# Kernel optimization log

Hardware: AMD Instinct MI355X
Metric: run time of the kernel (lower is better)

Reference implementation:

```python
import jax, jax.numpy as jnp
import numpy as np
from jax import lax
from jax.scipy.special import logsumexp

LOG2PI = 1.8378770664093453

def _gauss_lp(x, mean, logvar):
    return -0.5 * ((x - mean) ** 2 * jnp.exp(-logvar) + logvar + LOG2PI)

def setup_inputs() -> dict:
    key = jax.random.key(0)
    ks = jax.random.split(key, 12)
    B, T, D, H, X, K, U = 32, 1024, 512, 512, 32, 8, 2
    s = 0.05
    return {
        'ys': jax.random.normal(ks[0], (B, T, D), jnp.float32),
        'us': jax.random.normal(ks[1], (B, T, U), jnp.float32),
        'eps': jax.random.normal(ks[2], (B, T, X), jnp.float32),
        'W1': jax.random.normal(ks[3], (D, H), jnp.float32) * s,
        'b1': jnp.zeros((H,), jnp.float32),
        'Wmu': jax.random.normal(ks[4], (H, X), jnp.float32) * s,
        'bmu': jnp.zeros((X,), jnp.float32),
        'Wlv': jax.random.normal(ks[5], (H, X), jnp.float32) * s,
        'blv': jnp.zeros((X,), jnp.float32),
        'Wz': jax.random.normal(ks[6], (X, K * K), jnp.float32) * s,
        'bz': jnp.zeros((K * K,), jnp.float32),
        'A': jax.random.normal(ks[7], (K, X, X), jnp.float32) * s,
        'Bu': jax.random.normal(ks[8], (K, U, X), jnp.float32) * s,
        'bx': jnp.zeros((K, X), jnp.float32),
        'x_logvar': jnp.zeros((K, X), jnp.float32),
        'x0_mean': jax.random.normal(ks[9], (K, X), jnp.float32) * s,
        'x0_logvar': jnp.zeros((K, X), jnp.float32),
        'C': jax.random.normal(ks[10], (X, D), jnp.float32) * s,
        'd': jnp.zeros((D,), jnp.float32),
        'y_logvar': jnp.zeros((D,), jnp.float32),
        'log_init_z': jnp.zeros((K,), jnp.float32),
    }

def _forward_backward(log_a, log_b, log_init):
    # log_a: [B,T,K,K] with log_a[:,t,j,k] = log p(z_t=j | z_{t-1}=k); log_b: [B,T,K]
    B, T, K = log_b.shape
    la = jnp.moveaxis(log_a[:, 1:], 1, 0)  # [T-1,B,K,K]
    lb = jnp.moveaxis(log_b[:, 1:], 1, 0)  # [T-1,B,K]
    a0 = log_init[None, :] + log_b[:, 0]
    c0 = logsumexp(a0, axis=-1)
    a0 = a0 - c0[:, None]
    def fstep(alpha, ab):
        la_t, lb_t = ab
        a = lb_t + logsumexp(la_t + alpha[:, None, :], axis=-1)
        c = logsumexp(a, axis=-1)
        an = a - c[:, None]
        return an, (an, c)
    _, (alphas, cs) = lax.scan(fstep, a0, (la, lb))
    log_px = c0 + jnp.sum(cs, axis=0)  # [B] log marginal likelihood
    fwd = jnp.concatenate([a0[None], alphas], axis=0)  # [T,B,K]
    betaT = jnp.zeros((B, K), log_b.dtype)
    def bstep(beta, ab):
        la_t, lb_t = ab
        b = logsumexp(la_t + (lb_t + beta)[:, :, None], axis=1)  # sum over next-state j
        b = b - logsumexp(b, axis=-1, keepdims=True)
        return b, b
    _, betas = lax.scan(bstep, betaT, (la, lb), reverse=True)
    bwd = jnp.concatenate([betas, betaT[None]], axis=0)  # [T,B,K]
    lg = fwd + bwd
    log_gamma1 = lg - logsumexp(lg, axis=-1, keepdims=True)
    return jnp.moveaxis(log_gamma1, 0, 1), log_px

def reference(ys, us, eps, W1, b1, Wmu, bmu, Wlv, blv, Wz, bz, A, Bu, bx,
              x_logvar, x0_mean, x0_logvar, C, d, y_logvar, log_init_z):
    B, T, D = ys.shape
    K, X = x0_mean.shape
    # inference net q(x|y): per-step MLP producing Gaussian, reparameterized sample
    h = jnp.tanh(ys @ W1 + b1)
    mu = h @ Wmu + bmu
    lv = h @ Wlv + blv
    x = mu + jnp.exp(0.5 * lv) * eps                        # [B,T,X]
    x_entropy = 0.5 * jnp.sum(eps ** 2 + lv + LOG2PI, -1)   # -log q(x^), [B,T]
    # discrete transition log p(z_t | z_{t-1}, x_{t-1}) with log(eye) prepended at t=0
    logits = (x[:, :-1] @ Wz + bz).reshape(B, T - 1, K, K)
    log_a_t = jax.nn.log_softmax(logits, axis=-2)           # normalize_logprob axis=-2
    log_eye = jnp.log(jnp.eye(K, dtype=ys.dtype) + 1e-10)[None, None]
    log_a = jnp.concatenate([jnp.broadcast_to(log_eye, (B, 1, K, K)), log_a_t], axis=1)
    # continuous likelihood log p(x_t | x_{t-1}, u_t, z_t=k) -> [B,T,K]
    log_b0 = jnp.sum(_gauss_lp(x[:, 0, None, :], x0_mean, x0_logvar), -1)  # [B,K]
    means = (jnp.einsum('btd,kde->btke', x[:, :-1], A)
             + jnp.einsum('btu,kue->btke', us[:, 1:], Bu) + bx)            # [B,T-1,K,X]
    log_bt = jnp.sum(_gauss_lp(x[:, 1:, None, :], means, x_logvar), -1)
    log_b = jnp.concatenate([log_b0[:, None], log_bt], axis=1)
    log_init = jax.nn.log_softmax(log_init_z)
    log_gamma1, log_px = _forward_backward(log_a, log_b, log_init)
    # posterior-weighted generated mean mixed over states, then emission
    xt1_gen = jnp.sum(means * jnp.exp(log_gamma1[:, 1:, :, None]), axis=-2)
    x_gen1 = jnp.concatenate([x[:, :1], xt1_gen], axis=1)
    y_mean = x_gen1 @ C + d
    log_py = jnp.sum(_gauss_lp(ys, y_mean, y_logvar), -1)   # [B,T]
    log_p_xy = log_px + jnp.sum(log_py, -1)                 # [B]
    log_qx = jnp.mean(jnp.sum(x_entropy, 1))
    elbo = jnp.mean(log_p_xy) + log_qx
    return elbo
```

## Files before the change

### kernel.cpp

```cpp
#include <hip/hip_runtime.h>
#include <math.h>

#define LOG2PI 1.8378770664093453f

#define NB 32
#define NT 1024
#define ND 512
#define NH 512
#define NX 32
#define NK 8
#define NU 2

#define NCH 93
#define CHL 11

typedef __attribute__((ext_vector_type(8))) short bf16x8;
typedef __attribute__((ext_vector_type(4))) float f32x4;

__device__ __forceinline__ unsigned short f2bf(float f) {
    unsigned u = __float_as_uint(f);
    unsigned r = (u + 0x7FFF + ((u >> 16) & 1)) >> 16;
    return (unsigned short)r;
}

// ... 35 lines not shown
}

__device__ __forceinline__ float fb_matvecT(float4 a0, float4 a1, float w) {
    float q0 = a0.x * w;
    float t1 = dppx<DPP_X1>(a0.y * w);
    float t2 = dppx<DPP_X2>(a0.z * w);
    float t3 = dppx<DPP_X3>(a0.w * w);
    float t7 = dppx<DPP_X7>(a1.w * w);
    float t4 = dppx<DPP_X7>(dppx<DPP_X3>(a1.x * w));
    float t5 = dppx<DPP_X7>(dppx<DPP_X2>(a1.y * w));
    float t6 = dppx<DPP_X7>(dppx<DPP_X1>(a1.z * w));
    return ((q0 + t1) + (t2 + t3)) + ((t4 + t5) + (t6 + t7));
}

__device__ __forceinline__ float gsum8(float v) {
    float s = v + dppx<DPP_X1>(v);
    s = s + dppx<DPP_X2>(s);
    s = s + dppx<DPP_X7>(dppx<DPP_X3>(s));
    return s;
}

__device__ __forceinline__ float lse8_high(float v) {
    float m = v;
    m = fmaxf(m, __shfl_xor(m, 8, 64));
    m = fmaxf(m, __shfl_xor(m, 16, 64));
    m = fmaxf(m, __shfl_xor(m, 32, 64));
    float s = __expf(v - m);
    s += __shfl_xor(s, 8, 64);
    s += __shfl_xor(s, 16, 64);
    s += __shfl_xor(s, 32, 64);
    return m + __logf(s);
}

__global__ __launch_bounds__(256) void k_castT(
    const float* __restrict__ W, unsigned short* __restrict__ WT)
{
    __shared__ float tile[32][33];
    const int bx = blockIdx.x * 32;
    const int by = blockIdx.y * 32;
    const int tx = threadIdx.x & 31, ty = threadIdx.x >> 5;
    for (int i = ty; i < 32; i += 8)
        tile[i][tx] = W[(size_t)(bx + i) * 512 + by + tx];
    __syncthreads();
    for (int i = ty; i < 32; i += 8)
        WT[(size_t)(by + i) * 512 + bx + tx] = f2bf(tile[tx][i]);
}

__global__ __launch_bounds__(256) void k_cast_mulv(
    const float* __restrict__ Wmu, const float* __restrict__ Wlv,
    unsigned short* __restrict__ out)
{
    __shared__ float tile[32][33];
    const float* W = blockIdx.y ? Wlv : Wmu;
    const int base = blockIdx.y * 32;
    const int g = blockIdx.x;
    const int tx = threadIdx.x & 31, ty = threadIdx.x >> 5;
    for (int i = ty; i < 32; i += 8)
        tile[i][tx] = W[(size_t)(g * 32 + i) * 32 + tx];
    __syncthreads();
    for (int i = ty; i < 32; i += 8)
        out[(size_t)(base + i) * 512 + g * 32 + tx] = f2bf(tile[tx][i]);
}

__global__ __launch_bounds__(256) void k_prepc1(
    const float* __restrict__ ylv, float* __restrict__ ivbuf,
    float* __restrict__ term0)
{
    __shared__ float part[256];
    const int tid = threadIdx.x;
    float s = 0.f;
    for (int i = tid; i < 512; i += 256) {
        float lv = ylv[i];
        ivbuf[i] = expf(-lv);
        s += lv + LOG2PI;
    }
    part[tid] = s;
    __syncthreads();
    for (int st = 128; st; st >>= 1) {
        if (tid < st) part[tid] += part[tid + st];
        __syncthreads();
    }
    if (tid == 0) term0[0] = part[0];
}

__global__ __launch_bounds__(256) void k_prepc2(
    const float* __restrict__ C, const float* __restrict__ dvec,
    const float* __restrict__ ivbuf, unsigned short* __restrict__ W2bf,
    float* __restrict__ G, float* __restrict__ c2x)
{
    const int x = blockIdx.x;
    const int tid = threadIdx.x;
    if (x == 32) {
        for (int i = tid; i < 32 * 512; i += 256)
            W2bf[i] = f2bf(C[i] * ivbuf[i & 511]);
        return;
    }
    const int y = tid >> 3, seg = tid & 7;
    const float* Cx = &C[(size_t)x * 512];
    const float* Cy = &C[(size_t)y * 512];
    float p = 0.f;
    for (int j = 0; j < 64; ++j) {
        int dcol = seg * 64 + j;
        p = fmaf(Cx[dcol] * ivbuf[dcol], Cy[dcol], p);
    }
    p = gsum8(p);
    if (seg == 0) G[x * 33 + y] = p;
    if (tid < 8) {
        float q = 0.f;
        for (int j = 0; j < 64; ++j) {
            int dcol = tid * 64 + j;
            q = fmaf(Cx[dcol] * ivbuf[dcol], dvec[dcol], q);
        }
        q = gsum8(q);
        if (tid == 0) c2x[x] = q;
    }
}

__global__ __launch_bounds__(256) void k_cast_ys_t1(
    const float* __restrict__ ys, const float* __restrict__ dvec,
    const float* __restrict__ ivbuf, unsigned short* __restrict__ ysb,
    float* __restrict__ term1)
{
    const int tid = threadIdx.x;
    const int c8 = tid & 7;
    const int rbase = blockIdx.x * 128;
    float t1p[4] = {0.f, 0.f, 0.f, 0.f};
    for (int k0 = 0; k0 < 512; k0 += 64) {
        const float4 dv0 = *reinterpret_cast<const float4*>(&dvec[k0 + c8 * 8]);
        const float4 dv1 = *reinterpret_cast<const float4*>(&dvec[k0 + c8 * 8 + 4]);
        const float4 iv0 = *reinterpret_cast<const float4*>(&ivbuf[k0 + c8 * 8]);
        const float4 iv1 = *reinterpret_cast<const float4*>(&ivbuf[k0 + c8 * 8 + 4]);
#pragma unroll
        for (int r = 0; r < 4; ++r) {
            int row = rbase + (tid >> 3) + r * 32;
            const float4 f0 = *reinterpret_cast<const float4*>(
                &ys[(size_t)row * 512 + k0 + c8 * 8]);
            const float4 f1 = *reinterpret_cast<const float4*>(
                &ys[(size_t)row * 512 + k0 + c8 * 8 + 4]);
            float g0 = f0.x - dv0.x, g1 = f0.y - dv0.y;
            float g2 = f0.z - dv0.z, g3 = f0.w - dv0.w;
            float g4 = f1.x - dv1.x, g5 = f1.y - dv1.y;
            float g6 = f1.z - dv1.z, g7 = f1.w - dv1.w;
            t1p[r] += (g0 * g0 * iv0.x + g1 * g1 * iv0.y)
                    + (g2 * g2 * iv0.z + g3 * g3 * iv0.w)
                    + (g4 * g4 * iv1.x + g5 * g5 * iv1.y)
                    + (g6 * g6 * iv1.z + g7 * g7 * iv1.w);
            uint4 ua;
            ua.x = pack_bf2(f0.x, f0.y);
            ua.y = pack_bf2(f0.z, f0.w);
            ua.z = pack_bf2(f1.x, f1.y);
            ua.w = pack_bf2(f1.z, f1.w);
            *reinterpret_cast<uint4*>(&ysb[(size_t)row * 512 + k0 + c8 * 8]) = ua;
        }
    }
#pragma unroll
    for (int r = 0; r < 4; ++r) {
        float s = gsum8(t1p[r]);
        if ((tid & 7) == 0) term1[rbase + (tid >> 3) + r * 32] = s;
    }
}

__global__ __launch_bounds__(256) void k_mlp(
    const unsigned short* __restrict__ ysb,
    const unsigned short* __restrict__ W1T,
    const unsigned short* __restrict__ Wt,
    const unsigned short* __restrict__ W2bf,
    const float* __restrict__ b1,
    const float* __restrict__ bmu, const float* __restrict__ blv,
    const float* __restrict__ eps,
    float* __restrict__ x, float* __restrict__ xent,
    float* __restrict__ proj)
{
    __shared__ unsigned short SMEM[12288];
    unsigned short* As = SMEM;
    unsigned short* Bs = SMEM + 4096;
    const int tid = threadIdx.x;
    const int bm = blockIdx.x * 64;
    const int wid = tid >> 6, lane = tid & 63;
    const int wm = wid >> 1, wn = wid & 1;
    const int l15 = lane & 15, l16 = lane >> 4;

    f32x4 acc_mv[4];
    f32x4 acc_pj[2];
#pragma unroll
    for (int n = 0; n < 4; ++n) acc_mv[n] = (f32x4){0.f, 0.f, 0.f, 0.f};
#pragma unroll
    for (int n = 0; n < 2; ++n) acc_pj[n] = (f32x4){0.f, 0.f, 0.f, 0.f};

    for (int s = 0; s < 4; ++s) {
        const int bn = s * 128;
        f32x4 acc_h[2][4];
#pragma unroll
        for (int m = 0; m < 2; ++m)
#pragma unroll
            for (int n = 0; n < 4; ++n)
                acc_h[m][n] = (f32x4){0.f, 0.f, 0.f, 0.f};

        for (int k0 = 0; k0 < 512; k0 += 64) {
#pragma unroll
            for (int r = 0; r < 2; ++r) {
                int l = tid + r * 256;
                int row = l >> 3, c8 = l & 7;
                int sidx = row * 8 + (c8 ^ (row & 7));
                uint4 va = *reinterpret_cast<const uint4*>(
                    &ysb[(size_t)(bm + row) * 512 + k0 + c8 * 8]);
                *reinterpret_cast<uint4*>(&As[sidx * 8]) = va;
            }
#pragma unroll
            for (int r = 0; r < 4; ++r) {
                int l = tid + r * 256;
                int row = l >> 3, c8 = l & 7;
                int sidx = row * 8 + (c8 ^ (row & 7));
                uint4 vb = *reinterpret_cast<const uint4*>(
                    &W1T[(size_t)(bn + row) * 512 + k0 + c8 * 8]);
                *reinterpret_cast<uint4*>(&Bs[sidx * 8]) = vb;
            }
            __syncthreads();
#pragma unroll
            for (int kh = 0; kh < 2; ++kh) {
                const int c8r = kh * 4 + l16;
                bf16x8 af[2], bfr[4];
#pragma unroll
                for (int m = 0; m < 2; ++m) {
                    int rA = wm * 32 + m * 16 + l15;
                    af[m] = *reinterpret_cast<bf16x8*>(
                        &As[rA * 64 + (c8r ^ (rA & 7)) * 8]);
                }
#pragma unroll
                for (int n = 0; n < 4; ++n) {
                    int rB = wn * 64 + n * 16 + l15;
                    bfr[n] = *reinterpret_cast<bf16x8*>(
                        &Bs[rB * 64 + (c8r ^ (rB & 7)) * 8]);
                }
#pragma unroll
                for (int m = 0; m < 2; ++m)
#pragma unroll
                    for (int n = 0; n < 4; ++n)
                        acc_h[m][n] = __builtin_amdgcn_mfma_f32_16x16x32_bf16(
                            af[m], bfr[n], acc_h[m][n], 0, 0, 0);
                if (s == 0) {
#pragma unroll
                    for (int n2 = 0; n2 < 2; ++n2) {
                        bf16x8 b2 = *reinterpret_cast<const bf16x8*>(
                            &W2bf[(size_t)(n2 * 16 + l15) * 512 + k0 + c8r * 8]);
                        acc_pj[n2] = __builtin_amdgcn_mfma_f32_16x16x32_bf16(
                            af[wn], b2, acc_pj[n2], 0, 0, 0);
                    }
                }
            }
            __syncthreads();
        }
        float b1v[4];
#pragma unroll
        for (int n = 0; n < 4; ++n)
            b1v[n] = b1[bn + wn * 64 + n * 16 + l15];
#pragma unroll
        for (int m = 0; m < 2; ++m) {
#pragma unroll
            for (int q = 0; q < 4; ++q) {
                int row = wm * 32 + m * 16 + l16 * 4 + q;
#pragma unroll
                for (int n = 0; n < 4; ++n) {
                    int col = wn * 64 + n * 16 + l15;
                    float hv = tanh_fast(acc_h[m][n][q] + b1v[n]);
                    int slot = (col >> 3) ^ (row & 15);
                    SMEM[row * 128 + slot * 8 + (col & 7)] = f2bf(hv);
                }
            }
        }
        __syncthreads();
#pragma unroll
        for (int kh = 0; kh < 4; ++kh) {
            const int c8r = kh * 4 + l16;
            int rA = wid * 16 + l15;
            bf16x8 af2 = *reinterpret_cast<bf16x8*>(
                &SMEM[rA * 128 + (c8r ^ (rA & 15)) * 8]);
            bf16x8 bf2[4];
#pragma unroll
            for (int n = 0; n < 4; ++n) {
                int rB = n * 16 + l15;
                bf2[n] = *reinterpret_cast<const bf16x8*>(
                    &Wt[(size_t)rB * 512 + bn + c8r * 8]);
            }
#pragma unroll
            for (int n = 0; n < 4; ++n)
                acc_mv[n] = __builtin_amdgcn_mfma_f32_16x16x32_bf16(
                    af2, bf2[n], acc_mv[n], 0, 0, 0);
        }
        __syncthreads();
    }
#pragma unroll
    for (int q = 0; q < 4; ++q) {
        int row = bm + wm * 32 + wn * 16 + l16 * 4 + q;
        proj[(size_t)row * 32 + l15] = acc_pj[0][q];
        proj[(size_t)row * 32 + 16 + l15] = acc_pj[1][q];
    }
    const int o0 = l15, o1 = 16 + l15;
    const float bm0 = bmu[o0], bm1 = bmu[o1];
    const float bl0 = blv[o0], bl1 = blv[o1];
#pragma unroll
    for (int q = 0; q < 4; ++q) {
        int row = bm + wid * 16 + l16 * 4 + q;
        float mu0 = acc_mv[0][q] + bm0;
        float mu1 = acc_mv[1][q] + bm1;
        float lv0 = acc_mv[2][q] + bl0;
        float lv1 = acc_mv[3][q] + bl1;
        float e0 = eps[(size_t)row * 32 + o0];
        float e1 = eps[(size_t)row * 32 + o1];
        x[(size_t)row * 32 + o0] = mu0 + __expf(0.5f * lv0) * e0;
        x[(size_t)row * 32 + o1] = mu1 + __expf(0.5f * lv1) * e1;
        float pe = (e0 * e0 + lv0) + (e1 * e1 + lv1);
        pe += __shfl_xor(pe, 1, 64);
        pe += __shfl_xor(pe, 2, 64);
        pe += __shfl_xor(pe, 4, 64);
        pe += __shfl_xor(pe, 8, 64);
        if (l15 == 0) xent[row] = 0.5f * (pe + 32.f * LOG2PI);
    }
}

__global__ __launch_bounds__(256) void k_loga(
    const float* __restrict__ x, const float* __restrict__ Wz,
    const float* __restrict__ bz, float* __restrict__ ap1)
{
    __shared__ float xs[32][32];
    const int tid = threadIdx.x;
    const int lane = tid & 63;
    const int wv = tid >> 6;
    const int itemBase = blockIdx.x * 32;
    {
        int r = tid >> 3, cc = (tid & 7) * 4;
        int item = itemBase + r;
        int src = (item & (NT - 1)) ? item - 1 : item;
        *reinterpret_cast<float4*>(&xs[r][cc]) =
            *reinterpret_cast<const float4*>(&x[(size_t)src * 32 + cc]);
    }
    float wcol[32];
#pragma unroll
    for (int e = 0; e < 32; ++e) wcol[e] = Wz[e * 64 + lane];
    const float bzv = bz[lane];
    __syncthreads();
    const int j = lane >> 3, k = lane & 7;
    for (int i = wv; i < 32; i += 4) {
        int item = itemBase + i;
        if ((item & (NT - 1)) == 0) continue;
        float acc = bzv;
#pragma unroll
        for (int e = 0; e < 32; ++e) acc = fmaf(xs[i][e], wcol[e], acc);
        float lse = lse8_high(acc);
        ap1[(size_t)item * 64 + j * 8 + (j ^ k)] = __expf(acc - lse);
    }
}

__global__ __launch_bounds__(256) void k_means8(
    const float* __restrict__ x, const float* __restrict__ us,
    const float* __restrict__ A, const float* __restrict__ Bu,
    const float* __restrict__ bx, const float* __restrict__ x_logvar,
    float* __restrict__ log_b)
{
    __shared__ float As[8192];
    __shared__ float xs8[8][32];
    __shared__ float us8[8][2];
    const int tid = threadIdx.x;
    const int base = blockIdx.x * 8;
    for (int i = tid; i < 2048; i += 256)
        reinterpret_cast<float4*>(As)[i] =
            reinterpret_cast<const float4*>(A)[i];
    {
        int row = tid >> 5, xo = tid & 31;
        int item = base + row;
        int b = item / 1023, tm = item - b * 1023;
        xs8[row][xo] = x[((size_t)b * NT + tm) * 32 + xo];
        if (xo < 2) us8[row][xo] = us[((size_t)b * NT + tm + 1) * 2 + xo];
    }
    __syncthreads();
    const int k = tid >> 5, xo = tid & 31;
    const float bxv = bx[k * 32 + xo];
    const float bu0 = Bu[(k * 2 + 0) * 32 + xo];
    const float bu1 = Bu[(k * 2 + 1) * 32 + xo];
    const float lvv = x_logvar[k * 32 + xo];
    const float ivv = expf(-lvv);
    const float basev = lvv + LOG2PI;
    for (int i = 0; i < 8; ++i) {
        int item = base + i;
        int b = item / 1023, tm = item - b * 1023;
        float acc = fmaf(us8[i][0], bu0, fmaf(us8[i][1], bu1, bxv));
#pragma unroll 8
        for (int e = 0; e < 32; ++e)
            acc = fmaf(xs8[i][e], As[k * 1024 + e * 32 + xo], acc);
        float xv = x[((size_t)b * NT + tm + 1) * 32 + xo];
        float dd = xv - acc;
        float term = dd * dd * ivv + basev;
        for (int m = 16; m; m >>= 1) term += __shfl_down(term, m, 32);
        if (xo == 0)
            log_b[((size_t)b * NT + tm + 1) * 8 + k] = -0.5f * term;
    }
}

__global__ __launch_bounds__(256) void k_logb0(
    const float* __restrict__ x, const float* __restrict__ x0_mean,
    const float* __restrict__ x0_logvar, float* __restrict__ log_b)
{
    const int b = blockIdx.x;
    const int tid = threadIdx.x;
    const int k = tid >> 5, xo = tid & 31;
    float xv = x[((size_t)b * NT) * 32 + xo];
    float mm = x0_mean[k * 32 + xo];
    float lvv = x0_logvar[k * 32 + xo];
    float dd = xv - mm;
    float term = -0.5f * (dd * dd * expf(-lvv) + lvv + LOG2PI);
    for (int m = 16; m; m >>= 1) term += __shfl_down(term, m, 32);
    if (xo == 0) log_b[(size_t)b * NT * 8 + k] = term;
}

__global__ __launch_bounds__(256) void k_prep(
    const float* __restrict__ log_b, float* __restrict__ bexp,
    float* __restrict__ mbsum)
{
    __shared__ float part[256];
    const int b = blockIdx.x;
    const int tid = threadIdx.x;
    float msum = 0.f;
    for (int t = tid; t < NT; t += 256) {
        const float* lbp = &log_b[((size_t)b * NT + t) * 8];
        float4 l0 = *reinterpret_cast<const float4*>(lbp);
        float4 l1 = *reinterpret_cast<const float4*>(lbp + 4);
        float mm = fmaxf(fmaxf(fmaxf(l0.x, l0.y), fmaxf(l0.z, l0.w)),
                         fmaxf(fmaxf(l1.x, l1.y), fmaxf(l1.z, l1.w)));
        float4 e0, e1;
        e0.x = expf(l0.x - mm); e0.y = expf(l0.y - mm);
        e0.z = expf(l0.z - mm); e0.w = expf(l0.w - mm);
        e1.x = expf(l1.x - mm); e1.y = expf(l1.y - mm);
        e1.z = expf(l1.z - mm); e1.w = expf(l1.w - mm);
        float* bp = &bexp[((size_t)b * NT + t) * 8];
        *reinterpret_cast<float4*>(bp) = e0;
        *reinterpret_cast<float4*>(bp + 4) = e1;
        msum += mm;
    }
    part[tid] = msum;
    __syncthreads();
    for (int s = 128; s; s >>= 1) {
        if (tid < s) part[tid] += part[tid + s];
        __syncthreads();
    }
    if (tid == 0) mbsum[b] = part[0];
}

__global__ __launch_bounds__(256) void k_fbA(
    const float* __restrict__ ap1, const float* __restrict__ bexp,
    float* __restrict__ Pfx, float* __restrict__ sA)
{
    const int tid = threadIdx.x;
    const int wg = blockIdx.x * 4 + (tid >> 6);
    const int lane = tid & 63;
    const int b = wg / NCH;
    const int c = wg - b * NCH;
    const int j = lane >> 3, k = lane & 7;
    const float* ap = &ap1[(size_t)b * NT * 64];
    const float* be = &bexp[(size_t)b * NT * 8];
    int t = CHL * c + 1;
    float P = be[t * 8 + j] * ap[t * 64 + j * 8 + (j ^ k)];
    float sacc = 0.f;
    for (int i = 1; i < CHL; ++i) {
        ++t;
        float4 m0 = *reinterpret_cast<const float4*>(&ap[(size_t)t * 64 + j * 8]);
        float4 m1 = *reinterpret_cast<const float4*>(&ap[(size_t)t * 64 + j * 8 + 4]);
// ... 19 lines not shown
            mx = fmaxf(mx, __shfl_xor(mx, 16, 64));
            mx = fmaxf(mx, __shfl_xor(mx, 32, 64));
            mx = fmaxf(mx, 1e-30f);
            float r = __builtin_amdgcn_rcpf(mx);
            P *= r;
            sacc -= __logf(r);
        }
    }
    Pfx[((size_t)b * NCH + c) * 64 + j * 8 + (j ^ k)] = P;
    if (lane == 0) sA[b * NCH + c] = sacc;
}

__global__ __launch_bounds__(128) void k_fbB(
    const float* __restrict__ Pfx, const float* __restrict__ sA,
    const float* __restrict__ bexp, const float* __restrict__ mbsum,
    const float* __restrict__ log_init_z,
    float* __restrict__ alphaB, float* __restrict__ betaB,
    float* __restrict__ log_px)
{
    const int b = blockIdx.x;
    const int tid = threadIdx.x;
    const int wave = tid >> 6;
    const int lane = tid & 63;
    const int st = lane & 7;
    const float* pf = &Pfx[(size_t)b * NCH * 64];
    if (wave == 0) {
        float liv[8];
        float mz = -1e30f, sz = 0.f;
#pragma unroll
        for (int q = 0; q < 8; ++q) liv[q] = log_init_z[q];
#pragma unroll
        for (int q = 0; q < 8; ++q) mz = fmaxf(mz, liv[q]);
#pragma unroll
        for (int q = 0; q < 8; ++q) sz += expf(liv[q] - mz);
        float alpha = (expf(liv[st] - mz) / sz) * bexp[(size_t)b * NT * 8 + st];
        float logS = 0.f, sAsum = 0.f;
        {
            float s = fmaxf(gsum8(alpha), 1e-35f);
            logS += __logf(s);
            alpha *= __builtin_amdgcn_rcpf(s);
        }
        if (lane < 8) alphaB[((size_t)b * (NCH + 1)) * 8 + lane] = alpha;
        for (int c = 0; c < NCH; ++c) {
            float4 a0 = *reinterpret_cast<const float4*>(&pf[(size_t)c * 64 + st * 8]);
            float4 a1 = *reinterpret_cast<const float4*>(&pf[(size_t)c * 64 + st * 8 + 4]);
            alpha = fb_matvec(a0, a1, alpha);
            float s = fmaxf(gsum8(alpha), 1e-35f);
            logS += __logf(s);
            alpha *= __builtin_amdgcn_rcpf(s);
            sAsum += sA[b * NCH + c];
            if (lane < 8) alphaB[((size_t)b * (NCH + 1) + c + 1) * 8 + lane] = alpha;
        }
        if (lane == 0) log_px[b] = mbsum[b] + sAsum + logS;
    } else {
        float beta = 1.f;
        if (lane < 8) betaB[((size_t)b * (NCH + 1) + NCH) * 8 + lane] = 1.f;
        for (int c = NCH - 1; c >= 0; --c) {
            float4 a0 = *reinterpret_cast<const float4*>(&pf[(size_t)c * 64 + st * 8]);
            float4 a1 = *reinterpret_cast<const float4*>(&pf[(size_t)c * 64 + st * 8 + 4]);
            beta = fb_matvecT(a0, a1, beta);
            float s = fmaxf(gsum8(beta), 1e-35f);
            beta *= __builtin_amdgcn_rcpf(s);
            if (lane < 8) betaB[((size_t)b * (NCH + 1) + c) * 8 + lane] = beta;
        }
    }
}

__global__ __launch_bounds__(256) void k_fbC(
// ... 21 lines not shown
        alpha = fb_matvec(a0, a1, alpha) * bv;
        if (i == 5)
            alpha *= __builtin_amdgcn_rcpf(fmaxf(gsum8(alpha), 1e-35f));
        alphaS[g][i - 1][st] = alpha;
    }
    float beta = betaB[((size_t)b * (NCH + 1) + c + 1) * 8 + st];
#pragma unroll
    for (int i = CHL; i >= 1; --i) {
        int t = t0 + i;
        float gv = alphaS[g][i - 1][st] * beta;
        float s = fmaxf(gsum8(gv), 1e-35f);
        gamma[((size_t)b * NT + t) * 8 + st] = gv * __builtin_amdgcn_rcpf(s);
        float4 a0 = *reinterpret_cast<const float4*>(&ap[(size_t)t * 64 + st * 8]);
        float4 a1 = *reinterpret_cast<const float4*>(&ap[(size_t)t * 64 + st * 8 + 4]);
        float bv = be[(size_t)t * 8 + st];
        beta = fb_matvecT(a0, a1, beta * bv);
        if (i == 6)
            beta *= __builtin_amdgcn_rcpf(fmaxf(gsum8(beta), 1e-35f));
    }
    if (c == 0) {
        float a0v = alphaB[((size_t)b * (NCH + 1)) * 8 + st];
        float gv = a0v * beta;
        float s = fmaxf(gsum8(gv), 1e-35f);
        gamma[((size_t)b * NT) * 8 + st] = gv * __builtin_amdgcn_rcpf(s);
    }
}

__global__ __launch_bounds__(256) void k_py(
    const float* __restrict__ x, const float* __restrict__ us,
    const float* __restrict__ A, const float* __restrict__ Bu,
    const float* __restrict__ bx, const float* __restrict__ gamma,
    const float* __restrict__ proj, const float* __restrict__ term1,
    const float* __restrict__ Gm, const float* __restrict__ c2x,
    const float* __restrict__ term0, const float* __restrict__ xent,
    float* __restrict__ red)
{
    __shared__ float As[8192];
    __shared__ float Gs[32 * 33];
    __shared__ float c2s[32];
    __shared__ float xp8[8][32];
    __shared__ float gs[8][8];
    __shared__ float us8[8][2];
    __shared__ float xgS[8][32];
    const int tid = threadIdx.x;
    const int itemBase = blockIdx.x * 8;
    const int t0 = itemBase & (NT - 1);
    for (int i = tid; i < 2048; i += 256)
        reinterpret_cast<float4*>(As)[i] =
            reinterpret_cast<const float4*>(A)[i];
    for (int i = tid; i < 32 * 33; i += 256) Gs[i] = Gm[i];
    if (tid < 32) c2s[tid] = c2x[tid];
    {
        int it = tid >> 5, xo = tid & 31;
        int t = t0 + it;
        int item = itemBase + it;
        xp8[it][xo] = (t > 0) ? x[((size_t)item - 1) * 32 + xo] : 0.f;
        if (xo < 8) gs[it][xo] = (t > 0) ? gamma[(size_t)item * 8 + xo] : 0.f;
        if (xo < 2) us8[it][xo] = (t > 0) ? us[(size_t)item * 2 + xo] : 0.f;
    }
    __syncthreads();
    const int it = tid >> 5;
    const int xo = tid & 31;
    const int t = t0 + it;
    const int item = itemBase + it;
    float xg;
    if (t == 0) {
        xg = x[(size_t)item * 32 + xo];
    } else {
        xg = 0.f;
#pragma unroll
        for (int k = 0; k < 8; ++k) {
            float acc = bx[k * 32 + xo];
            acc = fmaf(us8[it][0], Bu[(k * 2 + 0) * 32 + xo], acc);
            acc = fmaf(us8[it][1], Bu[(k * 2 + 1) * 32 + xo], acc);
#pragma unroll 8
            for (int e = 0; e < 32; ++e)
                acc = fmaf(xp8[it][e], As[k * 1024 + e * 32 + xo], acc);
            xg = fmaf(gs[it][k], acc, xg);
        }
    }
    xgS[it][xo] = xg;
    __syncthreads();
    float gmv = 0.f;
#pragma unroll 8
    for (int y = 0; y < 32; ++y)
        gmv = fmaf(Gs[xo * 33 + y], xgS[it][y], gmv);
    float val = xg * (proj[(size_t)item * 32 + xo] - c2s[xo] - 0.5f * gmv);
    val += __shfl_xor(val, 1, 64);
    val += __shfl_xor(val, 2, 64);
    val += __shfl_xor(val, 4, 64);
    val += __shfl_xor(val, 8, 64);
    val += __shfl_xor(val, 16, 64);
    if (xo == 0)
        red[item] = -0.5f * (term1[item] + term0[0]) + val + xent[item];
}

__global__ __launch_bounds__(256) void k_final(
    const float* __restrict__ red, const float* __restrict__ log_px,
    float* __restrict__ out)
{
    __shared__ float ssum[4];
    float s = 0.f;
    for (int i = threadIdx.x; i < NB * NT; i += 256) s += red[i];
    if (threadIdx.x < NB) s += log_px[threadIdx.x];
#pragma unroll
    for (int m = 1; m < 64; m <<= 1) s += __shfl_xor(s, m, 64);
    if ((threadIdx.x & 63) == 0) ssum[threadIdx.x >> 6] = s;
    __syncthreads();
    if (threadIdx.x == 0)
        out[0] = (ssum[0] + ssum[1] + ssum[2] + ssum[3]) / (float)NB;
}

extern "C" void kernel_launch(void* const* d_in, const int* in_sizes, int n_in,
                              void* d_out, int out_size, void* d_ws,
                              size_t ws_size, hipStream_t stream)
{
    const float* ys        = (const float*)d_in[0];
    const float* us        = (const float*)d_in[1];
    const float* eps       = (const float*)d_in[2];
    const float* W1        = (const float*)d_in[3];
    const float* b1        = (const float*)d_in[4];
    const float* Wmu       = (const float*)d_in[5];
    const float* bmu       = (const float*)d_in[6];
    const float* Wlv       = (const float*)d_in[7];
    const float* blv       = (const float*)d_in[8];
    const float* Wz        = (const float*)d_in[9];
    const float* bz        = (const float*)d_in[10];
    const float* A         = (const float*)d_in[11];
    const float* Bu        = (const float*)d_in[12];
    const float* bx        = (const float*)d_in[13];
    const float* x_logvar  = (const float*)d_in[14];
    const float* x0_mean   = (const float*)d_in[15];
    const float* x0_logvar = (const float*)d_in[16];
    const float* C         = (const float*)d_in[17];
    const float* dv        = (const float*)d_in[18];
    const float* y_logvar  = (const float*)d_in[19];
    const float* log_init_z= (const float*)d_in[20];
    float* out = (float*)d_out;

    float* ws = (float*)d_ws;
    float* x      = ws;
    float* xent   = x + 1048576;
    float* ap1    = xent + 32768;
    float* bexp   = ap1 + 2097152;
    float* log_b  = bexp + 262144;
    float* ysb_f  = log_b + 262144;
    float* gam    = ysb_f + 8388608;
    float* log_px = gam + 262144;
    float* mbsum  = log_px + 32;
    float* red    = mbsum + 32;
    float* w1t_f  = red + 32768;
    float* wmlv_f = w1t_f + 131072;
    float* proj   = wmlv_f + 16384;
    float* term1  = proj + 1048576;
    float* ivbuf  = term1 + 32768;
    float* w2bf_f = ivbuf + 512;
    float* Gm     = w2bf_f + 8192;
    float* c2x    = Gm + 1056;
    float* term0  = c2x + 32;
    float* Pfx    = term0 + 1;
    float* sA     = Pfx + 190464;
    float* alphaB = sA + 2976;
    float* betaB  = alphaB + 24064;

    unsigned short* ysb  = (unsigned short*)ysb_f;
    unsigned short* w1t  = (unsigned short*)w1t_f;
    unsigned short* wmlv = (unsigned short*)wmlv_f;
    unsigned short* w2bf = (unsigned short*)w2bf_f;

    k_prepc1    <<<1, 256, 0, stream>>>(y_logvar, ivbuf, term0);
    k_cast_ys_t1<<<256, 256, 0, stream>>>(ys, dv, ivbuf, ysb, term1);
    k_castT     <<<dim3(16, 16), 256, 0, stream>>>(W1, w1t);
    k_cast_mulv <<<dim3(16, 2), 256, 0, stream>>>(Wmu, Wlv, wmlv);
    k_prepc2    <<<33, 256, 0, stream>>>(C, dv, ivbuf, w2bf, Gm, c2x);
    k_mlp       <<<512, 256, 0, stream>>>(ysb, w1t, wmlv, w2bf, b1, bmu, blv,
                                          eps, x, xent, proj);
    k_loga      <<<1024, 256, 0, stream>>>(x, Wz, bz, ap1);
    k_means8    <<<4092, 256, 0, stream>>>(x, us, A, Bu, bx, x_logvar, log_b);
    k_logb0     <<<32, 256, 0, stream>>>(x, x0_mean, x0_logvar, log_b);
    k_prep      <<<32, 256, 0, stream>>>(log_b, bexp, mbsum);
    k_fbA       <<<744, 256, 0, stream>>>(ap1, bexp, Pfx, sA);
    k_fbB       <<<32, 128, 0, stream>>>(Pfx, sA, bexp, mbsum, log_init_z,
                                         alphaB, betaB, log_px);
    k_fbC       <<<93, 256, 0, stream>>>(ap1, bexp, alphaB, betaB, gam);
    k_py        <<<4096, 256, 0, stream>>>(x, us, A, Bu, bx, gam, proj, term1,
                                           Gm, c2x, term0, xent, red);
    k_final     <<<1, 256, 0, stream>>>(red, log_px, out);
}
```

Before: 278.9 us.

## Fuse ys cast into MLP kernel and merge weight-prep and logb0 launches

The separate ys→bf16 cast pass is folded into the MLP kernel: each block reads its 64 fp32 rows once, computes term1 and writes a swizzled bf16 copy of the whole K=512 row into shared memory. The MLP then streams W1T fragments directly from global instead of staging both operands per k-tile. Weight-prep kernels are merged into one launch, logb0 is folded into the means kernel, and term0 moves into the final reduction, removing several launches and the 16 MB bf16 ys round trip. In exchange, the 80 KB of shared memory per block cuts occupancy, and the uncached global W1T loads may add latency.

```diff
diff --git a/kernel.cpp b/kernel.cpp
--- a/kernel.cpp
+++ b/kernel.cpp
@@ -91,76 +91,54 @@
     return m + __logf(s);
 }
 
-__global__ __launch_bounds__(256) void k_castT(
-    const float* __restrict__ W, unsigned short* __restrict__ WT)
+__global__ __launch_bounds__(256) void k_prep_w(
+    const float* __restrict__ W1, const float* __restrict__ Wmu,
+    const float* __restrict__ Wlv, const float* __restrict__ C,
+    const float* __restrict__ dvec, const float* __restrict__ ylv,
+    unsigned short* __restrict__ WT, unsigned short* __restrict__ wmlv,
+    unsigned short* __restrict__ W2bf, float* __restrict__ G,
+    float* __restrict__ c2x)
 {
     __shared__ float tile[32][33];
-    const int bx = blockIdx.x * 32;
-    const int by = blockIdx.y * 32;
-    const int tx = threadIdx.x & 31, ty = threadIdx.x >> 5;
-    for (int i = ty; i < 32; i += 8)
-        tile[i][tx] = W[(size_t)(bx + i) * 512 + by + tx];
-    __syncthreads();
-    for (int i = ty; i < 32; i += 8)
-        WT[(size_t)(by + i) * 512 + bx + tx] = f2bf(tile[tx][i]);
-}
-
-__global__ __launch_bounds__(256) void k_cast_mulv(
-    const float* __restrict__ Wmu, const float* __restrict__ Wlv,
-    unsigned short* __restrict__ out)
-{
-    __shared__ float tile[32][33];
-    const float* W = blockIdx.y ? Wlv : Wmu;
-    const int base = blockIdx.y * 32;
-    const int g = blockIdx.x;
-    const int tx = threadIdx.x & 31, ty = threadIdx.x >> 5;
-    for (int i = ty; i < 32; i += 8)
-        tile[i][tx] = W[(size_t)(g * 32 + i) * 32 + tx];
-    __syncthreads();
-    for (int i = ty; i < 32; i += 8)
-        out[(size_t)(base + i) * 512 + g * 32 + tx] = f2bf(tile[tx][i]);
-}
-
-__global__ __launch_bounds__(256) void k_prepc1(
-    const float* __restrict__ ylv, float* __restrict__ ivbuf,
-    float* __restrict__ term0)
-{
-    __shared__ float part[256];
-    const int tid = threadIdx.x;
-    float s = 0.f;
-    for (int i = tid; i < 512; i += 256) {
-        float lv = ylv[i];
-        ivbuf[i] = expf(-lv);
-        s += lv + LOG2PI;
-    }
-    part[tid] = s;
-    __syncthreads();
-    for (int st = 128; st; st >>= 1) {
-        if (tid < st) part[tid] += part[tid + st];
+    const int bid = blockIdx.x;
+    const int tid = threadIdx.x;
+    if (bid < 256) {
+        const int bx = (bid & 15) * 32;
+        const int by = (bid >> 4) * 32;
+        const int tx = tid & 31, ty = tid >> 5;
+        for (int i = ty; i < 32; i += 8)
+            tile[i][tx] = W1[(size_t)(bx + i) * 512 + by + tx];
         __syncthreads();
-    }
-    if (tid == 0) term0[0] = part[0];
-}
-
-__global__ __launch_bounds__(256) void k_prepc2(
-    const float* __restrict__ C, const float* __restrict__ dvec,
-    const float* __restrict__ ivbuf, unsigned short* __restrict__ W2bf,
-    float* __restrict__ G, float* __restrict__ c2x)
-{
-    const int x = blockIdx.x;
-    const int tid = threadIdx.x;
-    if (x == 32) {
+        for (int i = ty; i < 32; i += 8)
+            WT[(size_t)(by + i) * 512 + bx + tx] = f2bf(tile[tx][i]);
+        return;
+    }
+    if (bid < 288) {
+        const int t = bid - 256;
+        const float* W = (t >> 4) ? Wlv : Wmu;
+        const int base = (t >> 4) * 32;
+        const int g = t & 15;
+        const int tx = tid & 31, ty = tid >> 5;
+        for (int i = ty; i < 32; i += 8)
+            tile[i][tx] = W[(size_t)(g * 32 + i) * 32 + tx];
+        __syncthreads();
+        for (int i = ty; i < 32; i += 8)
+            wmlv[(size_t)(base + i) * 512 + g * 32 + tx] = f2bf(tile[tx][i]);
+        return;
+    }
+    if (bid == 320) {
         for (int i = tid; i < 32 * 512; i += 256)
-            W2bf[i] = f2bf(C[i] * ivbuf[i & 511]);
+            W2bf[i] = f2bf(C[i] * __expf(-ylv[i & 511]));
         return;
     }
+    const int x = bid - 288;
     const int y = tid >> 3, seg = tid & 7;
     const float* Cx = &C[(size_t)x * 512];
     const float* Cy = &C[(size_t)y * 512];
     float p = 0.f;
     for (int j = 0; j < 64; ++j) {
         int dcol = seg * 64 + j;
-        p = fmaf(Cx[dcol] * ivbuf[dcol], Cy[dcol], p);
+        p = fmaf(Cx[dcol] * __expf(-ylv[dcol]), Cy[dcol], p);
     }
     p = gsum8(p);
     if (seg == 0) G[x * 33 + y] = p;
@@ -168,189 +146,144 @@
         float q = 0.f;
         for (int j = 0; j < 64; ++j) {
             int dcol = tid * 64 + j;
-            q = fmaf(Cx[dcol] * ivbuf[dcol], dvec[dcol], q);
+            q = fmaf(Cx[dcol] * __expf(-ylv[dcol]), dvec[dcol], q);
         }
         q = gsum8(q);
         if (tid == 0) c2x[x] = q;
     }
 }
 
-__global__ __launch_bounds__(256) void k_cast_ys_t1(
-    const float* __restrict__ ys, const float* __restrict__ dvec,
-    const float* __restrict__ ivbuf, unsigned short* __restrict__ ysb,
-    float* __restrict__ term1)
-{
-    const int tid = threadIdx.x;
-    const int c8 = tid & 7;
-    const int rbase = blockIdx.x * 128;
-    float t1p[4] = {0.f, 0.f, 0.f, 0.f};
-    for (int k0 = 0; k0 < 512; k0 += 64) {
-        const float4 dv0 = *reinterpret_cast<const float4*>(&dvec[k0 + c8 * 8]);
-        const float4 dv1 = *reinterpret_cast<const float4*>(&dvec[k0 + c8 * 8 + 4]);
-        const float4 iv0 = *reinterpret_cast<const float4*>(&ivbuf[k0 + c8 * 8]);
-        const float4 iv1 = *reinterpret_cast<const float4*>(&ivbuf[k0 + c8 * 8 + 4]);
-#pragma unroll
-        for (int r = 0; r < 4; ++r) {
-            int row = rbase + (tid >> 3) + r * 32;
-            const float4 f0 = *reinterpret_cast<const float4*>(
-                &ys[(size_t)row * 512 + k0 + c8 * 8]);
-            const float4 f1 = *reinterpret_cast<const float4*>(
-                &ys[(size_t)row * 512 + k0 + c8 * 8 + 4]);
-            float g0 = f0.x - dv0.x, g1 = f0.y - dv0.y;
-            float g2 = f0.z - dv0.z, g3 = f0.w - dv0.w;
-            float g4 = f1.x - dv1.x, g5 = f1.y - dv1.y;
-            float g6 = f1.z - dv1.z, g7 = f1.w - dv1.w;
-            t1p[r] += (g0 * g0 * iv0.x + g1 * g1 * iv0.y)
-                    + (g2 * g2 * iv0.z + g3 * g3 * iv0.w)
-                    + (g4 * g4 * iv1.x + g5 * g5 * iv1.y)
-                    + (g6 * g6 * iv1.z + g7 * g7 * iv1.w);
-            uint4 ua;
-            ua.x = pack_bf2(f0.x, f0.y);
-            ua.y = pack_bf2(f0.z, f0.w);
-            ua.z = pack_bf2(f1.x, f1.y);
-            ua.w = pack_bf2(f1.z, f1.w);
-            *reinterpret_cast<uint4*>(&ysb[(size_t)row * 512 + k0 + c8 * 8]) = ua;
-        }
-    }
-#pragma unroll
-    for (int r = 0; r < 4; ++r) {
-        float s = gsum8(t1p[r]);
-        if ((tid & 7) == 0) term1[rbase + (tid >> 3) + r * 32] = s;
-    }
-}
-
-__global__ __launch_bounds__(256) void k_mlp(
-    const unsigned short* __restrict__ ysb,
+__global__ __launch_bounds__(256) void k_mlp2(
+    const float* __restrict__ ys,
     const unsigned short* __restrict__ W1T,
     const unsigned short* __restrict__ Wt,
     const unsigned short* __restrict__ W2bf,
     const float* __restrict__ b1,
     const float* __restrict__ bmu, const float* __restrict__ blv,
     const float* __restrict__ eps,
+    const float* __restrict__ dvec, const float* __restrict__ ylv,
     float* __restrict__ x, float* __restrict__ xent,
-    float* __restrict__ proj)
-{
-    __shared__ unsigned short SMEM[12288];
-    unsigned short* As = SMEM;
-    unsigned short* Bs = SMEM + 4096;
+    float* __restrict__ proj, float* __restrict__ term1)
+{
+    __shared__ unsigned short As[64 * 512];
+    __shared__ unsigned short Hs[64 * 128];
     const int tid = threadIdx.x;
     const int bm = blockIdx.x * 64;
     const int wid = tid >> 6, lane = tid & 63;
-    const int wm = wid >> 1, wn = wid & 1;
     const int l15 = lane & 15, l16 = lane >> 4;
 
+    const float4 dv0 = *reinterpret_cast<const float4*>(&dvec[lane * 8]);
+    const float4 dv1 = *reinterpret_cast<const float4*>(&dvec[lane * 8 + 4]);
+    const float4 yl0 = *reinterpret_cast<const float4*>(&ylv[lane * 8]);
+    const float4 yl1 = *reinterpret_cast<const float4*>(&ylv[lane * 8 + 4]);
+    float4 iv0, iv1;
+    iv0.x = __expf(-yl0.x); iv0.y = __expf(-yl0.y);
+    iv0.z = __expf(-yl0.z); iv0.w = __expf(-yl0.w);
+    iv1.x = __expf(-yl1.x); iv1.y = __expf(-yl1.y);
+    iv1.z = __expf(-yl1.z); iv1.w = __expf(-yl1.w);
+
+#pragma unroll
+    for (int r = 0; r < 16; ++r) {
+        const int row = r * 4 + wid;
+        const float4 f0 = *reinterpret_cast<const float4*>(
+            &ys[(size_t)(bm + row) * 512 + lane * 8]);
+        const float4 f1 = *reinterpret_cast<const float4*>(
+            &ys[(size_t)(bm + row) * 512 + lane * 8 + 4]);
+        float g0 = f0.x - dv0.x, g1 = f0.y - dv0.y;
+        float g2 = f0.z - dv0.z, g3 = f0.w - dv0.w;
+        float g4 = f1.x - dv1.x, g5 = f1.y - dv1.y;
+        float g6 = f1.z - dv1.z, g7 = f1.w - dv1.w;
+        float t1 = (g0 * g0 * iv0.x + g1 * g1 * iv0.y)
+                 + (g2 * g2 * iv0.z + g3 * g3 * iv0.w)
+                 + (g4 * g4 * iv1.x + g5 * g5 * iv1.y)
+                 + (g6 * g6 * iv1.z + g7 * g7 * iv1.w);
+#pragma unroll
+        for (int m = 1; m < 64; m <<= 1) t1 += __shfl_xor(t1, m, 64);
+        if (lane == 0) term1[bm + row] = t1;
+        uint4 ua;
+        ua.x = pack_bf2(f0.x, f0.y);
+        ua.y = pack_bf2(f0.z, f0.w);
+        ua.z = pack_bf2(f1.x, f1.y);
+        ua.w = pack_bf2(f1.z, f1.w);
+        const int sp = lane ^ (row & 15);
+        *reinterpret_cast<uint4*>(&As[row * 512 + sp * 8]) = ua;
+    }
+    __syncthreads();
+
+    const int rA = wid * 16 + l15;
+
+    f32x4 acc_pj[2];
+    acc_pj[0] = (f32x4){0.f, 0.f, 0.f, 0.f};
+    acc_pj[1] = (f32x4){0.f, 0.f, 0.f, 0.f};
+#pragma unroll
+    for (int ks = 0; ks < 16; ++ks) {
+        const int sp = (ks * 4 + l16) ^ l15;
+        bf16x8 af = *reinterpret_cast<bf16x8*>(&As[rA * 512 + sp * 8]);
+        const int kcol = ks * 32 + l16 * 8;
+#pragma unroll
+        for (int n2 = 0; n2 < 2; ++n2) {
+            bf16x8 b2 = *reinterpret_cast<const bf16x8*>(
+                &W2bf[(size_t)(n2 * 16 + l15) * 512 + kcol]);
+            acc_pj[n2] = __builtin_amdgcn_mfma_f32_16x16x32_bf16(
+                af, b2, acc_pj[n2], 0, 0, 0);
+        }
+    }
+
     f32x4 acc_mv[4];
-    f32x4 acc_pj[2];
 #pragma unroll
     for (int n = 0; n < 4; ++n) acc_mv[n] = (f32x4){0.f, 0.f, 0.f, 0.f};
-#pragma unroll
-    for (int n = 0; n < 2; ++n) acc_pj[n] = (f32x4){0.f, 0.f, 0.f, 0.f};
-
+
+#pragma unroll 1
     for (int s = 0; s < 4; ++s) {
         const int bn = s * 128;
-        f32x4 acc_h[2][4];
-#pragma unroll
-        for (int m = 0; m < 2; ++m)
-#pragma unroll
-            for (int n = 0; n < 4; ++n)
-                acc_h[m][n] = (f32x4){0.f, 0.f, 0.f, 0.f};
-
-        for (int k0 = 0; k0 < 512; k0 += 64) {
-#pragma unroll
-            for (int r = 0; r < 2; ++r) {
-                int l = tid + r * 256;
-                int row = l >> 3, c8 = l & 7;
-                int sidx = row * 8 + (c8 ^ (row & 7));
-                uint4 va = *reinterpret_cast<const uint4*>(
-                    &ysb[(size_t)(bm + row) * 512 + k0 + c8 * 8]);
-                *reinterpret_cast<uint4*>(&As[sidx * 8]) = va;
+        f32x4 acc_h[8];
+#pragma unroll
+        for (int n = 0; n < 8; ++n) acc_h[n] = (f32x4){0.f, 0.f, 0.f, 0.f};
+#pragma unroll
+        for (int ks = 0; ks < 16; ++ks) {
+            const int sp = (ks * 4 + l16) ^ l15;
+            bf16x8 af = *reinterpret_cast<bf16x8*>(&As[rA * 512 + sp * 8]);
+            const int kcol = ks * 32 + l16 * 8;
+#pragma unroll
+            for (int n = 0; n < 8; ++n) {
+                bf16x8 bf = *reinterpret_cast<const bf16x8*>(
+                    &W1T[(size_t)(bn + n * 16 + l15) * 512 + kcol]);
+                acc_h[n] = __builtin_amdgcn_mfma_f32_16x16x32_bf16(
+                    af, bf, acc_h[n], 0, 0, 0);
             }
-#pragma unroll
-            for (int r = 0; r < 4; ++r) {
-                int l = tid + r * 256;
-                int row = l >> 3, c8 = l & 7;
-                int sidx = row * 8 + (c8 ^ (row & 7));
-                uint4 vb = *reinterpret_cast<const uint4*>(
-                    &W1T[(size_t)(bn + row) * 512 + k0 + c8 * 8]);
-                *reinterpret_cast<uint4*>(&Bs[sidx * 8]) = vb;
+        }
+        __syncthreads();
+#pragma unroll
+        for (int n = 0; n < 8; ++n) {
+            const float b1v = b1[bn + n * 16 + l15];
+#pragma unroll
+            for (int q = 0; q < 4; ++q) {
+                const int row = wid * 16 + l16 * 4 + q;
+                const int col = n * 16 + l15;
+                const float hv = tanh_fast(acc_h[n][q] + b1v);
+                const int sp2 = (col >> 3) ^ (row & 15);
+                Hs[row * 128 + sp2 * 8 + (col & 7)] = f2bf(hv);
             }
-            __syncthreads();
-#pragma unroll
-            for (int kh = 0; kh < 2; ++kh) {
-                const int c8r = kh * 4 + l16;
-                bf16x8 af[2], bfr[4];
-#pragma unroll
-                for (int m = 0; m < 2; ++m) {
-                    int rA = wm * 32 + m * 16 + l15;
-                    af[m] = *reinterpret_cast<bf16x8*>(
-                        &As[rA * 64 + (c8r ^ (rA & 7)) * 8]);
-                }
-#pragma unroll
-                for (int n = 0; n < 4; ++n) {
-                    int rB = wn * 64 + n * 16 + l15;
-                    bfr[n] = *reinterpret_cast<bf16x8*>(
-                        &Bs[rB * 64 + (c8r ^ (rB & 7)) * 8]);
-                }
-#pragma unroll
-                for (int m = 0; m < 2; ++m)
-#pragma unroll
-                    for (int n = 0; n < 4; ++n)
-                        acc_h[m][n] = __builtin_amdgcn_mfma_f32_16x16x32_bf16(
-                            af[m], bfr[n], acc_h[m][n], 0, 0, 0);
-                if (s == 0) {
-#pragma unroll
-                    for (int n2 = 0; n2 < 2; ++n2) {
-                        bf16x8 b2 = *reinterpret_cast<const bf16x8*>(
-                            &W2bf[(size_t)(n2 * 16 + l15) * 512 + k0 + c8r * 8]);
-                        acc_pj[n2] = __builtin_amdgcn_mfma_f32_16x16x32_bf16(
-                            af[wn], b2, acc_pj[n2], 0, 0, 0);
-                    }
-                }
+        }
+        __syncthreads();
+#pragma unroll
+        for (int ks2 = 0; ks2 < 4; ++ks2) {
+            const int sp3 = (ks2 * 4 + l16) ^ l15;
+            bf16x8 af2 = *reinterpret_cast<bf16x8*>(&Hs[rA * 128 + sp3 * 8]);
+            const int kcol2 = bn + ks2 * 32 + l16 * 8;
+#pragma unroll
+            for (int n = 0; n < 4; ++n) {
+                bf16x8 b2 = *reinterpret_cast<const bf16x8*>(
+                    &Wt[(size_t)(n * 16 + l15) * 512 + kcol2]);
+                acc_mv[n] = __builtin_amdgcn_mfma_f32_16x16x32_bf16(
+                    af2, b2, acc_mv[n], 0, 0, 0);
             }
-            __syncthreads();
-        }
-        float b1v[4];
-#pragma unroll
-        for (int n = 0; n < 4; ++n)
-            b1v[n] = b1[bn + wn * 64 + n * 16 + l15];
-#pragma unroll
-        for (int m = 0; m < 2; ++m) {
-#pragma unroll
-            for (int q = 0; q < 4; ++q) {
-                int row = wm * 32 + m * 16 + l16 * 4 + q;
-#pragma unroll
-                for (int n = 0; n < 4; ++n) {
-                    int col = wn * 64 + n * 16 + l15;
-                    float hv = tanh_fast(acc_h[m][n][q] + b1v[n]);
-                    int slot = (col >> 3) ^ (row & 15);
-                    SMEM[row * 128 + slot * 8 + (col & 7)] = f2bf(hv);
-                }
-            }
-        }
-        __syncthreads();
-#pragma unroll
-        for (int kh = 0; kh < 4; ++kh) {
-            const int c8r = kh * 4 + l16;
-            int rA = wid * 16 + l15;
-            bf16x8 af2 = *reinterpret_cast<bf16x8*>(
-                &SMEM[rA * 128 + (c8r ^ (rA & 15)) * 8]);
-            bf16x8 bf2[4];
-#pragma unroll
-            for (int n = 0; n < 4; ++n) {
-                int rB = n * 16 + l15;
-                bf2[n] = *reinterpret_cast<const bf16x8*>(
-                    &Wt[(size_t)rB * 512 + bn + c8r * 8]);
-            }
-#pragma unroll
-            for (int n = 0; n < 4; ++n)
-                acc_mv[n] = __builtin_amdgcn_mfma_f32_16x16x32_bf16(
-                    af2, bf2[n], acc_mv[n], 0, 0, 0);
-        }
-        __syncthreads();
-    }
+        }
+    }
+
 #pragma unroll
     for (int q = 0; q < 4; ++q) {
-        int row = bm + wm * 32 + wn * 16 + l16 * 4 + q;
+        const int row = bm + wid * 16 + l16 * 4 + q;
         proj[(size_t)row * 32 + l15] = acc_pj[0][q];
         proj[(size_t)row * 32 + 16 + l15] = acc_pj[1][q];
     }
@@ -359,7 +292,7 @@
     const float bl0 = blv[o0], bl1 = blv[o1];
 #pragma unroll
     for (int q = 0; q < 4; ++q) {
-        int row = bm + wid * 16 + l16 * 4 + q;
+        const int row = bm + wid * 16 + l16 * 4 + q;
         float mu0 = acc_mv[0][q] + bm0;
         float mu1 = acc_mv[1][q] + bm1;
         float lv0 = acc_mv[2][q] + bl0;
@@ -410,16 +343,29 @@
     }
 }
 
-__global__ __launch_bounds__(256) void k_means8(
+__global__ __launch_bounds__(256) void k_means8m(
     const float* __restrict__ x, const float* __restrict__ us,
     const float* __restrict__ A, const float* __restrict__ Bu,
     const float* __restrict__ bx, const float* __restrict__ x_logvar,
+    const float* __restrict__ x0_mean, const float* __restrict__ x0_logvar,
     float* __restrict__ log_b)
 {
     __shared__ float As[8192];
     __shared__ float xs8[8][32];
     __shared__ float us8[8][2];
     const int tid = threadIdx.x;
+    if (blockIdx.x >= 4092) {
+        const int b = blockIdx.x - 4092;
+        const int k = tid >> 5, xo = tid & 31;
+        float xv = x[((size_t)b * NT) * 32 + xo];
+        float mm = x0_mean[k * 32 + xo];
+        float lvv = x0_logvar[k * 32 + xo];
+        float dd = xv - mm;
+        float term = -0.5f * (dd * dd * __expf(-lvv) + lvv + LOG2PI);
+        for (int m = 16; m; m >>= 1) term += __shfl_down(term, m, 32);
+        if (xo == 0) log_b[(size_t)b * NT * 8 + k] = term;
+        return;
+    }
     const int base = blockIdx.x * 8;
     for (int i = tid; i < 2048; i += 256)
         reinterpret_cast<float4*>(As)[i] =
@@ -437,7 +383,7 @@
     const float bu0 = Bu[(k * 2 + 0) * 32 + xo];
     const float bu1 = Bu[(k * 2 + 1) * 32 + xo];
     const float lvv = x_logvar[k * 32 + xo];
-    const float ivv = expf(-lvv);
+    const float ivv = __expf(-lvv);
     const float basev = lvv + LOG2PI;
     for (int i = 0; i < 8; ++i) {
         int item = base + i;
@@ -455,22 +401,6 @@
     }
 }
 
-__global__ __launch_bounds__(256) void k_logb0(
-    const float* __restrict__ x, const float* __restrict__ x0_mean,
-    const float* __restrict__ x0_logvar, float* __restrict__ log_b)
-{
-    const int b = blockIdx.x;
-    const int tid = threadIdx.x;
-    const int k = tid >> 5, xo = tid & 31;
-    float xv = x[((size_t)b * NT) * 32 + xo];
-    float mm = x0_mean[k * 32 + xo];
-    float lvv = x0_logvar[k * 32 + xo];
-    float dd = xv - mm;
-    float term = -0.5f * (dd * dd * expf(-lvv) + lvv + LOG2PI);
-    for (int m = 16; m; m >>= 1) term += __shfl_down(term, m, 32);
-    if (xo == 0) log_b[(size_t)b * NT * 8 + k] = term;
-}
-
 __global__ __launch_bounds__(256) void k_prep(
     const float* __restrict__ log_b, float* __restrict__ bexp,
     float* __restrict__ mbsum)
@@ -486,10 +416,10 @@
         float mm = fmaxf(fmaxf(fmaxf(l0.x, l0.y), fmaxf(l0.z, l0.w)),
                          fmaxf(fmaxf(l1.x, l1.y), fmaxf(l1.z, l1.w)));
         float4 e0, e1;
-        e0.x = expf(l0.x - mm); e0.y = expf(l0.y - mm);
-        e0.z = expf(l0.z - mm); e0.w = expf(l0.w - mm);
-        e1.x = expf(l1.x - mm); e1.y = expf(l1.y - mm);
-        e1.z = expf(l1.z - mm); e1.w = expf(l1.w - mm);
+        e0.x = __expf(l0.x - mm); e0.y = __expf(l0.y - mm);
+        e0.z = __expf(l0.z - mm); e0.w = __expf(l0.w - mm);
+        e1.x = __expf(l1.x - mm); e1.y = __expf(l1.y - mm);
+        e1.z = __expf(l1.z - mm); e1.w = __expf(l1.w - mm);
         float* bp = &bexp[((size_t)b * NT + t) * 8];
         *reinterpret_cast<float4*>(bp) = e0;
         *reinterpret_cast<float4*>(bp + 4) = e1;
@@ -575,8 +505,8 @@
 #pragma unroll
         for (int q = 0; q < 8; ++q) mz = fmaxf(mz, liv[q]);
 #pragma unroll
-        for (int q = 0; q < 8; ++q) sz += expf(liv[q] - mz);
-        float alpha = (expf(liv[st] - mz) / sz) * bexp[(size_t)b * NT * 8 + st];
+        for (int q = 0; q < 8; ++q) sz += __expf(liv[q] - mz);
+        float alpha = (__expf(liv[st] - mz) / sz) * bexp[(size_t)b * NT * 8 + st];
         float logS = 0.f, sAsum = 0.f;
         {
             float s = fmaxf(gsum8(alpha), 1e-35f);
@@ -664,8 +594,7 @@
     const float* __restrict__ bx, const float* __restrict__ gamma,
     const float* __restrict__ proj, const float* __restrict__ term1,
     const float* __restrict__ Gm, const float* __restrict__ c2x,
-    const float* __restrict__ term0, const float* __restrict__ xent,
-    float* __restrict__ red)
+    const float* __restrict__ xent, float* __restrict__ red)
 {
     __shared__ float As[8192];
     __shared__ float Gs[32 * 33];
@@ -724,23 +653,32 @@
     val += __shfl_xor(val, 8, 64);
     val += __shfl_xor(val, 16, 64);
     if (xo == 0)
-        red[item] = -0.5f * (term1[item] + term0[0]) + val + xent[item];
+        red[item] = -0.5f * term1[item] + val + xent[item];
 }
 
 __global__ __launch_bounds__(256) void k_final(
     const float* __restrict__ red, const float* __restrict__ log_px,
-    float* __restrict__ out)
+    const float* __restrict__ ylv, float* __restrict__ out)
 {
     __shared__ float ssum[4];
-    float s = 0.f;
-    for (int i = threadIdx.x; i < NB * NT; i += 256) s += red[i];
-    if (threadIdx.x < NB) s += log_px[threadIdx.x];
-#pragma unroll
-    for (int m = 1; m < 64; m <<= 1) s += __shfl_xor(s, m, 64);
-    if ((threadIdx.x & 63) == 0) ssum[threadIdx.x >> 6] = s;
+    __shared__ float ssum2[4];
+    const int tid = threadIdx.x;
+    float s = 0.f, t = 0.f;
+    for (int i = tid; i < NB * NT; i += 256) s += red[i];
+    if (tid < NB) s += log_px[tid];
+    for (int i = tid; i < 512; i += 256) t += ylv[i] + LOG2PI;
+#pragma unroll
+    for (int m = 1; m < 64; m <<= 1) {
+        s += __shfl_xor(s, m, 64);
+        t += __shfl_xor(t, m, 64);
+    }
+    if ((tid & 63) == 0) { ssum[tid >> 6] = s; ssum2[tid >> 6] = t; }
     __syncthreads();
-    if (threadIdx.x == 0)
-        out[0] = (ssum[0] + ssum[1] + ssum[2] + ssum[3]) / (float)NB;
+    if (tid == 0) {
+        float S = ssum[0] + ssum[1] + ssum[2] + ssum[3];
+        float T = ssum2[0] + ssum2[1] + ssum2[2] + ssum2[3];
+        out[0] = S / (float)NB - 512.0f * T;
+    }
 }
 
 extern "C" void kernel_launch(void* const* d_in, const int* in_sizes, int n_in,
@@ -776,8 +714,7 @@
     float* ap1    = xent + 32768;
     float* bexp   = ap1 + 2097152;
     float* log_b  = bexp + 262144;
-    float* ysb_f  = log_b + 262144;
-    float* gam    = ysb_f + 8388608;
+    float* gam    = log_b + 262144;
     float* log_px = gam + 262144;
     float* mbsum  = log_px + 32;
     float* red    = mbsum + 32;
@@ -785,37 +722,31 @@
     float* wmlv_f = w1t_f + 131072;
     float* proj   = wmlv_f + 16384;
     float* term1  = proj + 1048576;
-    float* ivbuf  = term1 + 32768;
-    float* w2bf_f = ivbuf + 512;
+    float* w2bf_f = term1 + 32768;
     float* Gm     = w2bf_f + 8192;
     float* c2x    = Gm + 1056;
-    float* term0  = c2x + 32;
-    float* Pfx    = term0 + 1;
+    float* Pfx    = c2x + 32;
     float* sA     = Pfx + 190464;
     float* alphaB = sA + 2976;
     float* betaB  = alphaB + 24064;
 
-    unsigned short* ysb  = (unsigned short*)ysb_f;
     unsigned short* w1t  = (unsigned short*)w1t_f;
     unsigned short* wmlv = (unsigned short*)wmlv_f;
     unsigned short* w2bf = (unsigned short*)w2bf_f;
 
-    k_prepc1    <<<1, 256, 0, stream>>>(y_logvar, ivbuf, term0);
-    k_cast_ys_t1<<<256, 256, 0, stream>>>(ys, dv, ivbuf, ysb, term1);
-    k_castT     <<<dim3(16, 16), 256, 0, stream>>>(W1, w1t);
-    k_cast_mulv <<<dim3(16, 2), 256, 0, stream>>>(Wmu, Wlv, wmlv);
-    k_prepc2    <<<33, 256, 0, stream>>>(C, dv, ivbuf, w2bf, Gm, c2x);
-    k_mlp       <<<512, 256, 0, stream>>>(ysb, w1t, wmlv, w2bf, b1, bmu, blv,
-                                          eps, x, xent, proj);
-    k_loga      <<<1024, 256, 0, stream>>>(x, Wz, bz, ap1);
-    k_means8    <<<4092, 256, 0, stream>>>(x, us, A, Bu, bx, x_logvar, log_b);
-    k_logb0     <<<32, 256, 0, stream>>>(x, x0_mean, x0_logvar, log_b);
-    k_prep      <<<32, 256, 0, stream>>>(log_b, bexp, mbsum);
-    k_fbA       <<<744, 256, 0, stream>>>(ap1, bexp, Pfx, sA);
-    k_fbB       <<<32, 128, 0, stream>>>(Pfx, sA, bexp, mbsum, log_init_z,
-                                         alphaB, betaB, log_px);
-    k_fbC       <<<93, 256, 0, stream>>>(ap1, bexp, alphaB, betaB, gam);
-    k_py        <<<4096, 256, 0, stream>>>(x, us, A, Bu, bx, gam, proj, term1,
-                                           Gm, c2x, term0, xent, red);
-    k_final     <<<1, 256, 0, stream>>>(red, log_px, out);
-}
+    k_prep_w  <<<321, 256, 0, stream>>>(W1, Wmu, Wlv, C, dv, y_logvar,
+                                        w1t, wmlv, w2bf, Gm, c2x);
+    k_mlp2    <<<512, 256, 0, stream>>>(ys, w1t, wmlv, w2bf, b1, bmu, blv,
+                                        eps, dv, y_logvar, x, xent, proj, term1);
+    k_loga    <<<1024, 256, 0, stream>>>(x, Wz, bz, ap1);
+    k_means8m <<<4124, 256, 0, stream>>>(x, us, A, Bu, bx, x_logvar,
+                                         x0_mean, x0_logvar, log_b);
+    k_prep    <<<32, 256, 0, stream>>>(log_b, bexp, mbsum);
+    k_fbA     <<<744, 256, 0, stream>>>(ap1, bexp, Pfx, sA);
+    k_fbB     <<<32, 128, 0, stream>>>(Pfx, sA, bexp, mbsum, log_init_z,
+                                       alphaB, betaB, log_px);
+    k_fbC     <<<93, 256, 0, stream>>>(ap1, bexp, alphaB, betaB, gam);
+    k_py      <<<4096, 256, 0, stream>>>(x, us, A, Bu, bx, gam, proj, term1,
+                                         Gm, c2x, xent, red);
+    k_final   <<<1, 256, 0, stream>>>(red, log_px, y_logvar, out);
+}
```

After: 463.7 us. +66.2%, slower.
